# Kernel tuning notes

Hardware: AMD Instinct MI355X
Metric: run time of the kernel (lower is better)

Reference implementation:

```python
import jax, jax.numpy as jnp
import numpy as np

SMOOTH = 6.0
EPS = 1e-8
NEG_SLOPE = 0.1

def setup_inputs() -> dict:
    key = jax.random.key(0)
    k1, k2 = jax.random.split(key)
    im = jax.random.normal(k1, (8192, 1024), dtype=jnp.float32)
    aud = jax.random.normal(k2, (8192, 1024), dtype=jnp.float32)
    return {"im": im, "aud": aud}

def _l2norm(x, dim=1):
    norm = jnp.sqrt(jnp.sum(x * x, axis=dim, keepdims=True)) + EPS
    return x / norm

def reference(im, aud):
    # scores: [N, M]
    scores = im @ aud.T
    s = jax.nn.leaky_relu(scores, NEG_SLOPE)
    # row path: l2norm over dim=1, scaled softmax over last dim
    s1 = jax.nn.softmax(_l2norm(s, dim=1) * SMOOTH, axis=-1)          # [N, M]
    # col path: transpose, l2norm over dim=1 (rows of [M, N]), softmax
    s2 = jax.nn.softmax(_l2norm(s.T, dim=1) * SMOOTH, axis=-1)        # [M, N]
    im_rec = s1 @ aud   # [N, D]
    aud_rec = s2 @ im   # [M, D]
    return (im_rec, aud_rec)
```

## Files before the change

### kernel.cpp

```cpp
#include <hip/hip_runtime.h>
#include <stdint.h>
#include <stddef.h>

#define NTOK 8192
#define DDIM 1024

#define WS_F 202375168ull
#define WS_C2048 135266304ull
#define WS_C1024 101711872ull
#define WS_C512   84934656ull

using f16   = _Float16;
using f16x8 = __attribute__((ext_vector_type(8))) _Float16;
using f32x4 = __attribute__((ext_vector_type(4))) float;

__device__ __forceinline__ void gload16(const void* g, void* l) {
  __builtin_amdgcn_global_load_lds(
      (const __attribute__((address_space(1))) void*)g,
      (__attribute__((address_space(3))) void*)l, 16, 0, 0);
}

__device__ __forceinline__ void stage_tile(const f16* __restrict__ src, int ld,
                                           int row0, int k0, f16* lds, int tid) {
#pragma unroll
  for (int base = 0; base < 1024; base += 256) {
    const int cl = base + tid;
    const int r = cl >> 3;
    const int cs = (cl & 7) ^ (r & 7);
    gload16(src + (size_t)(row0 + r) * ld + k0 + cs * 8, (char*)lds + (size_t)cl * 16);
  }
}

__device__ __forceinline__ f16x8 frag_ld(const f16* lds, int r, int kc) {
  const int c = kc ^ (r & 7);
  return *(const f16x8*)((const char*)lds + r * 128 + c * 16);
}

__device__ __forceinline__ int xcd_swz(int bid, int nwg) {
  return (bid & 7) * (nwg >> 3) + (bid >> 3);
}

__global__ void prep_kernel(const float* __restrict__ inA, const float* __restrict__ inB,
                            f16* __restrict__ nA, f16* __restrict__ tA,
                            f16* __restrict__ nB, f16* __restrict__ tB) {
  const float* in = blockIdx.z ? inB : inA;
  f16* nrm = blockIdx.z ? nB : nA;
  f16* trp = blockIdx.z ? tB : tA;
  __shared__ float tile[32][33];
  const int c0 = blockIdx.x * 32;
  const int r0 = blockIdx.y * 32;
  const int tx = threadIdx.x, ty = threadIdx.y;
#pragma unroll
  for (int rr = 0; rr < 32; rr += 8) {
    const int r = r0 + rr + ty;
    const float v = in[(size_t)r * DDIM + c0 + tx];
    tile[rr + ty][tx] = v;
    nrm[(size_t)r * DDIM + c0 + tx] = (f16)v;
  }
  __syncthreads();
#pragma unroll
  for (int rr = 0; rr < 32; rr += 8) {
    trp[(size_t)(c0 + rr + ty) * NTOK + r0 + tx] = (f16)tile[tx][rr + ty];
  }
}

#define GEMM_CORE_R(Asrc, lda, Bsrc, ldb, K0, K1)                                     \
  for (int k0 = (K0); k0 < (K1); k0 += 64) {                                          \
    __syncthreads();                                                                  \
    stage_tile(Asrc, lda, row0, k0, Al, tid);                                         \
    stage_tile(Bsrc, ldb, col0, k0, Bl, tid);                                         \
    __syncthreads();                                                                  \
    _Pragma("unroll")                                                                 \
    for (int kk = 0; kk < 2; ++kk) {                                                  \
      f16x8 a[4], b[4];                                                               \
      _Pragma("unroll")                                                               \
      for (int m = 0; m < 4; ++m) a[m] = frag_ld(Al, wr + m * 16 + l15, kk * 4 + lg); \
      _Pragma("unroll")                                                               \
      for (int n = 0; n < 4; ++n) b[n] = frag_ld(Bl, wc + n * 16 + l15, kk * 4 + lg); \
      _Pragma("unroll")                                                               \
      for (int m = 0; m < 4; ++m)                                                     \
        _Pragma("unroll")                                                             \
        for (int n = 0; n < 4; ++n)                                                   \
          acc[m][n] = __builtin_amdgcn_mfma_f32_16x16x32_f16(a[m], b[n], acc[m][n], 0, 0, 0); \
    }                                                                                 \
  }
#define GEMM_CORE(Asrc, lda, Bsrc, ldb, KLEN) GEMM_CORE_R(Asrc, lda, Bsrc, ldb, 0, KLEN)

__global__ __launch_bounds__(256, 2)
void sgemm_kernel(const f16* __restrict__ A, const f16* __restrict__ B,
                  float* __restrict__ row_ss, float* __restrict__ col_ss,
                  f16* __restrict__ Sb) {
  __shared__ __align__(16) char smem[128 * 136 * 2];
  f16* Al = (f16*)smem;
  f16* Bl = (f16*)(smem + 16384);
  f16* RP = (f16*)smem;
  const int tid = threadIdx.x;
  const int lane = tid & 63, wid = tid >> 6;
  const int wr = (wid >> 1) * 64, wc = (wid & 1) * 64;
  const int l15 = lane & 15, lg = lane >> 4;
  const int swz = xcd_swz(blockIdx.x, 4096);
  const int row0 = (swz & 63) * 128, col0 = (swz >> 6) * 128;
  f32x4 acc[4][4];
#pragma unroll
  for (int m = 0; m < 4; ++m)
#pragma unroll
    for (int n = 0; n < 4; ++n) acc[m][n] = (f32x4){0.f, 0.f, 0.f, 0.f};

  GEMM_CORE(A, DDIM, B, DDIM, DDIM)

#pragma unroll
  for (int m = 0; m < 4; ++m)
#pragma unroll
    for (int n = 0; n < 4; ++n)
#pragma unroll
      for (int q = 0; q < 4; ++q) {
        const float v = acc[m][n][q];
        acc[m][n][q] = v > 0.f ? v : 0.1f * v;
      }
  float cpart[4] = {0.f, 0.f, 0.f, 0.f};
#pragma unroll
  for (int m = 0; m < 4; ++m) {
    float rpart[4] = {0.f, 0.f, 0.f, 0.f};
#pragma unroll
    for (int n = 0; n < 4; ++n) {
#pragma unroll
      for (int q = 0; q < 4; ++q) {
        const float v2 = acc[m][n][q] * acc[m][n][q];
        rpart[q] += v2;
        cpart[n] += v2;
      }
    }
#pragma unroll
    for (int q = 0; q < 4; ++q) {
      float s = rpart[q];
      s += __shfl_xor(s, 1, 64);
      s += __shfl_xor(s, 2, 64);
      s += __shfl_xor(s, 4, 64);
      s += __shfl_xor(s, 8, 64);
      if (l15 == 0) atomicAdd(&row_ss[row0 + wr + m * 16 + lg * 4 + q], s);
    }
  }
#pragma unroll
  for (int n = 0; n < 4; ++n) {
    float s = cpart[n];
    s += __shfl_xor(s, 16, 64);
    s += __shfl_xor(s, 32, 64);
    if (lg == 0) atomicAdd(&col_ss[col0 + wc + n * 16 + l15], s);
  }
  __syncthreads();
#pragma unroll
  for (int m = 0; m < 4; ++m)
#pragma unroll
    for (int n = 0; n < 4; ++n)
#pragma unroll
      for (int q = 0; q < 4; ++q)
        RP[(wr + m * 16 + lg * 4 + q) * 136 + wc + n * 16 + l15] = (f16)acc[m][n][q];
  __syncthreads();
#pragma unroll
  for (int it = 0; it < 8; ++it) {
    const int r = it * 16 + (tid >> 4);
    const int c8 = (tid & 15) * 8;
    *(f16x8*)(Sb + (size_t)(row0 + r) * NTOK + col0 + c8) = *(const f16x8*)(RP + r * 136 + c8);
  }
}

__global__ void scales_kernel(const float* __restrict__ row_ss, const float* __restrict__ col_ss,
                              float* __restrict__ s1p, float* __restrict__ s2p) {
  const int i = blockIdx.x * 256 + threadIdx.x;
  const float c = 6.0f * 1.4426950408889634f;
  s1p[i] = c / (sqrtf(row_ss[i]) + 1e-8f);
  s2p[i] = c / (sqrtf(col_ss[i]) + 1e-8f);
}

__global__ __launch_bounds__(256)
void texp_kernel(const f16* __restrict__ Sb, f16* __restrict__ P2c,
                 const float* __restrict__ s2p, float* __restrict__ Z2, int j0c) {
  __shared__ float T[128][33];
  const int t = threadIdx.x;
  const int i0 = blockIdx.x * 128;
  const int jc = blockIdx.y * 32;
  const int jg = j0c + jc;
#pragma unroll
  for (int it = 0; it < 2; ++it) {
    const int lin = it * 256 + t;
    const int r = lin >> 2, c8 = (lin & 3) * 8;
    const f16x8 v = *(const f16x8*)(Sb + (size_t)(i0 + r) * NTOK + jg + c8);
#pragma unroll
    for (int e = 0; e < 8; ++e) T[r][c8 + e] = (float)v[e];
  }
  __syncthreads();
#pragma unroll
  for (int it = 0; it < 2; ++it) {
    const int lin = it * 256 + t;
    const int j = lin >> 4, ic = lin & 15;
    const float s = s2p[jg + j];
    f16x8 o;
    float sum = 0.f;
#pragma unroll
    for (int e = 0; e < 8; ++e) {
      const float p = exp2f(T[ic * 8 + e][j] * s);
      o[e] = (f16)p;
      sum += (float)o[e];
    }
    *(f16x8*)(P2c + (size_t)(jc + j) * NTOK + i0 + ic * 8) = o;
    sum += __shfl_xor(sum, 1, 64);
    sum += __shfl_xor(sum, 2, 64);
    sum += __shfl_xor(sum, 4, 64);
    sum += __shfl_xor(sum, 8, 64);
    if ((t & 15) == 0) atomicAdd(&Z2[jg + j], sum);
  }
}

__global__ __launch_bounds__(256, 2)
void gemm2_kernel(const f16* __restrict__ A, const f16* __restrict__ Bt,
                  float* __restrict__ C) {
  __shared__ __align__(16) f16 Al[128 * 64];
  __shared__ __align__(16) f16 Bl[128 * 64];
  const int tid = threadIdx.x;
  const int lane = tid & 63, wid = tid >> 6;
  const int wr = (wid >> 1) * 64, wc = (wid & 1) * 64;
  const int l15 = lane & 15, lg = lane >> 4;
  const int swz = xcd_swz(blockIdx.x, 512);
  const int tile = swz >> 2, kq = swz & 3;
  const int row0 = (tile >> 3) * 128, col0 = (tile & 7) * 128;
  f32x4 acc[4][4];
#pragma unroll
  for (int m = 0; m < 4; ++m)
#pragma unroll
    for (int n = 0; n < 4; ++n) acc[m][n] = (f32x4){0.f, 0.f, 0.f, 0.f};

  GEMM_CORE_R(A, NTOK, Bt, NTOK, kq * 2048, kq * 2048 + 2048)

#pragma unroll
  for (int m = 0; m < 4; ++m)
#pragma unroll
    for (int n = 0; n < 4; ++n) {
      const int ccol = col0 + wc + n * 16 + l15;
#pragma unroll
      for (int q = 0; q < 4; ++q) {
        const int crow = row0 + wr + m * 16 + lg * 4 + q;
        atomicAdd(&C[(size_t)crow * DDIM + ccol], acc[m][n][q]);
      }
    }
}

__global__ __launch_bounds__(256, 8)
void expz_kernel(f16* __restrict__ M, const float* __restrict__ s1p, float* __restrict__ Z1) {
  const int wid = threadIdx.x >> 6, lane = threadIdx.x & 63;
  const int row = blockIdx.x * 4 + wid;
  const float s = s1p[row];
  f16* rp = M + (size_t)row * NTOK;
  float acc = 0.f;
#pragma unroll
  for (int c = 0; c < 16; ++c) {
    f16x8* p = (f16x8*)(rp + (c * 64 + lane) * 8);
    f16x8 v = *p;
    f16x8 o;
#pragma unroll
    for (int e = 0; e < 8; ++e) {
      o[e] = (f16)exp2f((float)v[e] * s);
      acc += (float)o[e];
    }
    *p = o;
  }
#pragma unroll
  for (int d = 1; d < 64; d <<= 1) acc += __shfl_xor(acc, d, 64);
  if (lane == 0) Z1[row] = acc;
}

__global__ __launch_bounds__(256, 2)
void pass1_kernel(const f16* __restrict__ A, const f16* __restrict__ B,
                  float* __restrict__ row_ss, float* __restrict__ col_ss) {
  __shared__ __align__(16) f16 Al[128 * 64];
  __shared__ __align__(16) f16 Bl[128 * 64];
  const int tid = threadIdx.x;
  const int lane = tid & 63, wid = tid >> 6;
  const int wr = (wid >> 1) * 64, wc = (wid & 1) * 64;
  const int l15 = lane & 15, lg = lane >> 4;
  const int swz = xcd_swz(blockIdx.x, 4096);
  const int row0 = (swz & 63) * 128, col0 = (swz >> 6) * 128;
  f32x4 acc[4][4];
#pragma unroll
  for (int m = 0; m < 4; ++m)
#pragma unroll
    for (int n = 0; n < 4; ++n) acc[m][n] = (f32x4){0.f, 0.f, 0.f, 0.f};

  GEMM_CORE(A, DDIM, B, DDIM, DDIM)

  float cpart[4] = {0.f, 0.f, 0.f, 0.f};
#pragma unroll
  for (int m = 0; m < 4; ++m) {
    float rpart[4] = {0.f, 0.f, 0.f, 0.f};
#pragma unroll
    for (int n = 0; n < 4; ++n) {
#pragma unroll
      for (int q = 0; q < 4; ++q) {
        float v = acc[m][n][q];
        v = v > 0.f ? v : 0.1f * v;
        const float v2 = v * v;
        rpart[q] += v2;
        cpart[n] += v2;
      }
    }
#pragma unroll
    for (int q = 0; q < 4; ++q) {
      float s = rpart[q];
      s += __shfl_xor(s, 1, 64);
      s += __shfl_xor(s, 2, 64);
      s += __shfl_xor(s, 4, 64);
      s += __shfl_xor(s, 8, 64);
      if (l15 == 0) atomicAdd(&row_ss[row0 + wr + m * 16 + lg * 4 + q], s);
    }
  }
#pragma unroll
  for (int n = 0; n < 4; ++n) {
    float s = cpart[n];
    s += __shfl_xor(s, 16, 64);
    s += __shfl_xor(s, 32, 64);
    if (lg == 0) atomicAdd(&col_ss[col0 + wc + n * 16 + l15], s);
  }
}

__global__ __launch_bounds__(256, 2)
void pass2c_kernel(const f16* __restrict__ A, const f16* __restrict__ B,
                   const float* __restrict__ s1p, const float* __restrict__ s2p,
                   f16* __restrict__ P1c, f16* __restrict__ P2c,
                   float* __restrict__ Z1, float* __restrict__ Z2, int j0, int CHJ) {
  __shared__ __align__(16) char smem[128 * 136 * 2];
  f16* Al = (f16*)smem;
  f16* Bl = (f16*)(smem + 16384);
  f16* RP = (f16*)smem;
  const int tid = threadIdx.x;
  const int lane = tid & 63, wid = tid >> 6;
  const int wr = (wid >> 1) * 64, wc = (wid & 1) * 64;
  const int l15 = lane & 15, lg = lane >> 4;
  const int row0 = blockIdx.x * 128;
  const int col0loc = blockIdx.y * 128;
  const int col0 = j0 + col0loc;
  f32x4 acc[4][4];
#pragma unroll
  for (int m = 0; m < 4; ++m)
#pragma unroll
    for (int n = 0; n < 4; ++n) acc[m][n] = (f32x4){0.f, 0.f, 0.f, 0.f};

  GEMM_CORE(A, DDIM, B, DDIM, DDIM)

#pragma unroll
  for (int m = 0; m < 4; ++m)
#pragma unroll
    for (int n = 0; n < 4; ++n)
#pragma unroll
      for (int q = 0; q < 4; ++q) {
        const float v = acc[m][n][q];
        acc[m][n][q] = v > 0.f ? v : 0.1f * v;
      }
  float sr[4][4], sc[4];
#pragma unroll
  for (int m = 0; m < 4; ++m)
#pragma unroll
    for (int q = 0; q < 4; ++q) sr[m][q] = s1p[row0 + wr + m * 16 + lg * 4 + q];
#pragma unroll
  for (int n = 0; n < 4; ++n) sc[n] = s2p[col0 + wc + n * 16 + l15];

  __syncthreads();
#pragma unroll
  for (int m = 0; m < 4; ++m)
#pragma unroll
    for (int n = 0; n < 4; ++n)
#pragma unroll
      for (int q = 0; q < 4; ++q) {
        const float p = exp2f(acc[m][n][q] * sr[m][q]);
        RP[(wr + m * 16 + lg * 4 + q) * 136 + wc + n * 16 + l15] = (f16)p;
      }
  __syncthreads();
#pragma unroll
  for (int it = 0; it < 8; ++it) {
    const int r = it * 16 + (tid >> 4);
    const int c8 = (tid & 15) * 8;
    const f16x8 v = *(const f16x8*)(RP + r * 136 + c8);
    float s = 0.f;
#pragma unroll
    for (int e = 0; e < 8; ++e) s += (float)v[e];
    *(f16x8*)(P1c + (size_t)(row0 + r) * CHJ + col0loc + c8) = v;
    s += __shfl_xor(s, 1, 64);
    s += __shfl_xor(s, 2, 64);
    s += __shfl_xor(s, 4, 64);
    s += __shfl_xor(s, 8, 64);
    if ((tid & 15) == 0) atomicAdd(&Z1[row0 + r], s);
  }
  __syncthreads();
#pragma unroll
  for (int m = 0; m < 4; ++m)
#pragma unroll
    for (int n = 0; n < 4; ++n)
#pragma unroll
      for (int q = 0; q < 4; ++q) {
        const float p = exp2f(acc[m][n][q] * sc[n]);
        RP[(wc + n * 16 + l15) * 136 + wr + m * 16 + lg * 4 + q] = (f16)p;
      }
  __syncthreads();
#pragma unroll
  for (int it = 0; it < 8; ++it) {
    const int r = it * 16 + (tid >> 4);
    const int c8 = (tid & 15) * 8;
    const f16x8 v = *(const f16x8*)(RP + r * 136 + c8);
    float s = 0.f;
#pragma unroll
    for (int e = 0; e < 8; ++e) s += (float)v[e];
    *(f16x8*)(P2c + (size_t)(col0loc + r) * NTOK + row0 + c8) = v;
    s += __shfl_xor(s, 1, 64);
    s += __shfl_xor(s, 2, 64);
    s += __shfl_xor(s, 4, 64);
    s += __shfl_xor(s, 8, 64);
    if ((tid & 15) == 0) atomicAdd(&Z2[col0 + r], s);
  }
}

__global__ __launch_bounds__(256, 2)
void gemm_out_kernel(const f16* __restrict__ A, int lda,
                     const f16* __restrict__ Bt, int ldb,
                     float* __restrict__ C, int K, int beta, int nwg) {
  __shared__ __align__(16) f16 Al[128 * 64];
  __shared__ __align__(16) f16 Bl[128 * 64];
  const int tid = threadIdx.x;
  const int lane = tid & 63, wid = tid >> 6;
  const int wr = (wid >> 1) * 64, wc = (wid & 1) * 64;
  const int l15 = lane & 15, lg = lane >> 4;
  const int swz = xcd_swz(blockIdx.x, nwg);
  const int row0 = (swz >> 3) * 128, col0 = (swz & 7) * 128;
  f32x4 acc[4][4];
#pragma unroll
  for (int m = 0; m < 4; ++m)
#pragma unroll
    for (int n = 0; n < 4; ++n) acc[m][n] = (f32x4){0.f, 0.f, 0.f, 0.f};

  GEMM_CORE(A, lda, Bt, ldb, K)

#pragma unroll
  for (int m = 0; m < 4; ++m)
#pragma unroll
    for (int n = 0; n < 4; ++n) {
      const int ccol = col0 + wc + n * 16 + l15;
#pragma unroll
      for (int q = 0; q < 4; ++q) {
        const int crow = row0 + wr + m * 16 + lg * 4 + q;
        const size_t idx = (size_t)crow * DDIM + ccol;
        const float v = acc[m][n][q];
        C[idx] = beta ? C[idx] + v : v;
      }
    }
}

__global__ void norm_kernel(float* __restrict__ out, const float* __restrict__ Z1,
                            const float* __restrict__ Z2) {
  const size_t idx = (size_t)blockIdx.x * 256 + threadIdx.x;
  const size_t e = idx * 4;
  const size_t half = (size_t)NTOK * DDIM;
  const float* Z = (e < half) ? Z1 : Z2;
  const int r = (int)((e >> 10) & (NTOK - 1));
  const float inv = 1.0f / Z[r];
  f32x4* o = (f32x4*)out;
  f32x4 v = o[idx];
  v.x *= inv; v.y *= inv; v.z *= inv; v.w *= inv;
  o[idx] = v;
}

__global__ void fill_kernel(float* __restrict__ out, float v, size_t n) {
  const size_t i = (size_t)blockIdx.x * 256 + threadIdx.x;
  if (i < n) out[i] = v;
}

extern "C" void kernel_launch(void* const* d_in, const int* in_sizes, int n_in,
                              void* d_out, int out_size, void* d_ws, size_t ws_size,
                              hipStream_t stream) {
  const float* im = (const float*)d_in[0];
  const float* aud = (const float*)d_in[1];
  float* out = (float*)d_out;
  char* ws = (char*)d_ws;

  f16* im_h  = (f16*)(ws);
  f16* aud_h = (f16*)(ws + (size_t)16777216);
  f16* imT   = (f16*)(ws + (size_t)33554432);
  f16* audT  = (f16*)(ws + (size_t)50331648);
  float* row_ss = (float*)(ws + (size_t)67108864);
  float* col_ss = (float*)(ws + (size_t)67108864 + 32768);
  float* Z1     = (float*)(ws + (size_t)67108864 + 65536);
  float* Z2     = (float*)(ws + (size_t)67108864 + 98304);
  float* s1p    = (float*)(ws + (size_t)67108864 + 131072);
  float* s2p    = (float*)(ws + (size_t)67108864 + 163840);

  if (ws_size >= WS_F) {
    f16* Sb  = (f16*)(ws + (size_t)68157440);
    f16* P2c = (f16*)(ws);

    hipMemsetAsync(row_ss, 0, 2 * NTOK * sizeof(float), stream);
    hipMemsetAsync(Z2, 0, NTOK * sizeof(float), stream);
    hipMemsetAsync(out + (size_t)NTOK * DDIM, 0, (size_t)NTOK * DDIM * 4, stream);
    prep_kernel<<<dim3(32, 256, 2), dim3(32, 8), 0, stream>>>(im, aud, im_h, imT, aud_h, audT);
    sgemm_kernel<<<4096, 256, 0, stream>>>(im_h, aud_h, row_ss, col_ss, Sb);
    scales_kernel<<<NTOK / 256, 256, 0, stream>>>(row_ss, col_ss, s1p, s2p);
    for (int c = 0; c < 4; ++c) {
      const int j0c = c * 2048;
      texp_kernel<<<dim3(64, 64), 256, 0, stream>>>(Sb, P2c, s2p, Z2, j0c);
      gemm2_kernel<<<512, 256, 0, stream>>>(P2c, imT,
                                            out + (size_t)NTOK * DDIM + (size_t)j0c * DDIM);
    }
    expz_kernel<<<NTOK / 4, 256, 0, stream>>>(Sb, s1p, Z1);
    gemm_out_kernel<<<512, 256, 0, stream>>>(Sb, NTOK, audT, NTOK, out, NTOK, 0, 512);
    norm_kernel<<<16384, 256, 0, stream>>>(out, Z1, Z2);
  } else if (ws_size >= WS_C512) {
    const int CHJ = (ws_size >= WS_C2048) ? 2048 : (ws_size >= WS_C1024) ? 1024 : 512;
    f16* P1c = (f16*)(ws + (size_t)68157440);
    f16* P2c = (f16*)(ws + (size_t)68157440 + (size_t)NTOK * CHJ * 2);

    hipMemsetAsync(row_ss, 0, 2 * NTOK * sizeof(float), stream);
    hipMemsetAsync(Z1, 0, NTOK * sizeof(float), stream);
    hipMemsetAsync(Z2, 0, NTOK * sizeof(float), stream);
    prep_kernel<<<dim3(32, 256, 2), dim3(32, 8), 0, stream>>>(im, aud, im_h, imT, aud_h, audT);
    pass1_kernel<<<4096, 256, 0, stream>>>(im_h, aud_h, row_ss, col_ss);
    scales_kernel<<<NTOK / 256, 256, 0, stream>>>(row_ss, col_ss, s1p, s2p);
    const int nchunk = NTOK / CHJ;
    for (int cj = 0; cj < nchunk; ++cj) {
      const int j0 = cj * CHJ;
      pass2c_kernel<<<dim3(64, CHJ / 128), 256, 0, stream>>>(im_h, aud_h, s1p, s2p, P1c, P2c,
                                                             Z1, Z2, j0, CHJ);
      gemm_out_kernel<<<512, 256, 0, stream>>>(P1c, CHJ, audT + j0, NTOK, out, CHJ, cj > 0, 512);
      gemm_out_kernel<<<(CHJ / 128) * 8, 256, 0, stream>>>(P2c, NTOK, imT, NTOK,
                                                           out + (size_t)NTOK * DDIM +
                                                               (size_t)j0 * DDIM,
                                                           NTOK, 0, (CHJ / 128) * 8);
    }
    norm_kernel<<<16384, 256, 0, stream>>>(out, Z1, Z2);
  } else {
    fill_kernel<<<(2u * NTOK * DDIM + 255) / 256, 256, 0, stream>>>(out, 1234.5f,
                                                                    (size_t)2 * NTOK * DDIM);
  }
}
```

Before: 842.6 us.

## Fuse row exp into transpose-exp kernel and fold normalization into GEMM epilogues

```diff
diff --git a/kernel.cpp b/kernel.cpp
--- a/kernel.cpp
+++ b/kernel.cpp
@@ -173,47 +173,64 @@
 }
 
 __global__ __launch_bounds__(256)
-void texp_kernel(const f16* __restrict__ Sb, f16* __restrict__ P2c,
-                 const float* __restrict__ s2p, float* __restrict__ Z2, int j0c) {
-  __shared__ float T[128][33];
+void texp2_kernel(f16* __restrict__ Sb, f16* __restrict__ P2c,
+                  const float* __restrict__ s1p, const float* __restrict__ s2p,
+                  float* __restrict__ Z1, float* __restrict__ Z2, int j0c) {
+  __shared__ f16 T[64][130];
   const int t = threadIdx.x;
   const int i0 = blockIdx.x * 128;
-  const int jc = blockIdx.y * 32;
-  const int jg = j0c + jc;
-#pragma unroll
-  for (int it = 0; it < 2; ++it) {
+  const int jl = blockIdx.y * 64;
+  const int jg = j0c + jl;
+#pragma unroll
+  for (int it = 0; it < 4; ++it) {
     const int lin = it * 256 + t;
-    const int r = lin >> 2, c8 = (lin & 3) * 8;
-    const f16x8 v = *(const f16x8*)(Sb + (size_t)(i0 + r) * NTOK + jg + c8);
-#pragma unroll
-    for (int e = 0; e < 8; ++e) T[r][c8 + e] = (float)v[e];
-  }
-  __syncthreads();
-#pragma unroll
-  for (int it = 0; it < 2; ++it) {
+    const int r = lin >> 3;
+    const int c8 = (lin & 7) * 8;
+    f16* addr = Sb + (size_t)(i0 + r) * NTOK + jg + c8;
+    const f16x8 v = *(const f16x8*)addr;
+    const float s1 = s1p[i0 + r];
+    f16x8 o;
+    float zp = 0.f;
+#pragma unroll
+    for (int e = 0; e < 8; ++e) {
+      const float x = (float)v[e];
+      T[c8 + e][r] = v[e];
+      o[e] = (f16)exp2f(x * s1);
+      zp += (float)o[e];
+    }
+    *(f16x8*)addr = o;
+    zp += __shfl_xor(zp, 1, 64);
+    zp += __shfl_xor(zp, 2, 64);
+    zp += __shfl_xor(zp, 4, 64);
+    if ((t & 7) == 0) atomicAdd(&Z1[i0 + r], zp);
+  }
+  __syncthreads();
+#pragma unroll
+  for (int it = 0; it < 4; ++it) {
     const int lin = it * 256 + t;
-    const int j = lin >> 4, ic = lin & 15;
-    const float s = s2p[jg + j];
+    const int jj = lin >> 4;
+    const int iof = (lin & 15) * 8;
+    const float s2 = s2p[jg + jj];
     f16x8 o;
-    float sum = 0.f;
+    float zp = 0.f;
 #pragma unroll
     for (int e = 0; e < 8; ++e) {
-      const float p = exp2f(T[ic * 8 + e][j] * s);
-      o[e] = (f16)p;
-      sum += (float)o[e];
-    }
-    *(f16x8*)(P2c + (size_t)(jc + j) * NTOK + i0 + ic * 8) = o;
-    sum += __shfl_xor(sum, 1, 64);
-    sum += __shfl_xor(sum, 2, 64);
-    sum += __shfl_xor(sum, 4, 64);
-    sum += __shfl_xor(sum, 8, 64);
-    if ((t & 15) == 0) atomicAdd(&Z2[jg + j], sum);
+      const float x = (float)T[jj][iof + e];
+      o[e] = (f16)exp2f(x * s2);
+      zp += (float)o[e];
+    }
+    *(f16x8*)(P2c + (size_t)(jl + jj) * NTOK + i0 + iof) = o;
+    zp += __shfl_xor(zp, 1, 64);
+    zp += __shfl_xor(zp, 2, 64);
+    zp += __shfl_xor(zp, 4, 64);
+    zp += __shfl_xor(zp, 8, 64);
+    if ((t & 15) == 0) atomicAdd(&Z2[jg + jj], zp);
   }
 }
 
 __global__ __launch_bounds__(256, 2)
 void gemm2_kernel(const f16* __restrict__ A, const f16* __restrict__ Bt,
-                  float* __restrict__ C) {
+                  float* __restrict__ C, const float* __restrict__ Zrow) {
   __shared__ __align__(16) f16 Al[128 * 64];
   __shared__ __align__(16) f16 Bl[128 * 64];
   const int tid = threadIdx.x;
@@ -239,33 +256,9 @@
 #pragma unroll
       for (int q = 0; q < 4; ++q) {
         const int crow = row0 + wr + m * 16 + lg * 4 + q;
-        atomicAdd(&C[(size_t)crow * DDIM + ccol], acc[m][n][q]);
-      }
-    }
-}
-
-__global__ __launch_bounds__(256, 8)
-void expz_kernel(f16* __restrict__ M, const float* __restrict__ s1p, float* __restrict__ Z1) {
-  const int wid = threadIdx.x >> 6, lane = threadIdx.x & 63;
-  const int row = blockIdx.x * 4 + wid;
-  const float s = s1p[row];
-  f16* rp = M + (size_t)row * NTOK;
-  float acc = 0.f;
-#pragma unroll
-  for (int c = 0; c < 16; ++c) {
-    f16x8* p = (f16x8*)(rp + (c * 64 + lane) * 8);
-    f16x8 v = *p;
-    f16x8 o;
-#pragma unroll
-    for (int e = 0; e < 8; ++e) {
-      o[e] = (f16)exp2f((float)v[e] * s);
-      acc += (float)o[e];
-    }
-    *p = o;
-  }
-#pragma unroll
-  for (int d = 1; d < 64; d <<= 1) acc += __shfl_xor(acc, d, 64);
-  if (lane == 0) Z1[row] = acc;
+        atomicAdd(&C[(size_t)crow * DDIM + ccol], acc[m][n][q] / Zrow[crow]);
+      }
+    }
 }
 
 __global__ __launch_bounds__(256, 2)
@@ -419,7 +412,8 @@
 __global__ __launch_bounds__(256, 2)
 void gemm_out_kernel(const f16* __restrict__ A, int lda,
                      const f16* __restrict__ Bt, int ldb,
-                     float* __restrict__ C, int K, int beta, int nwg) {
+                     float* __restrict__ C, int K, int beta, int nwg,
+                     const float* __restrict__ Zrow) {
   __shared__ __align__(16) f16 Al[128 * 64];
   __shared__ __align__(16) f16 Bl[128 * 64];
   const int tid = threadIdx.x;
@@ -445,7 +439,8 @@
       for (int q = 0; q < 4; ++q) {
         const int crow = row0 + wr + m * 16 + lg * 4 + q;
         const size_t idx = (size_t)crow * DDIM + ccol;
-        const float v = acc[m][n][q];
+        float v = acc[m][n][q];
+        if (Zrow) v /= Zrow[crow];
         C[idx] = beta ? C[idx] + v : v;
       }
     }
@@ -494,28 +489,26 @@
     f16* P2c = (f16*)(ws);
 
     hipMemsetAsync(row_ss, 0, 2 * NTOK * sizeof(float), stream);
-    hipMemsetAsync(Z2, 0, NTOK * sizeof(float), stream);
+    hipMemsetAsync(Z1, 0, 2 * NTOK * sizeof(float), stream);
     hipMemsetAsync(out + (size_t)NTOK * DDIM, 0, (size_t)NTOK * DDIM * 4, stream);
     prep_kernel<<<dim3(32, 256, 2), dim3(32, 8), 0, stream>>>(im, aud, im_h, imT, aud_h, audT);
     sgemm_kernel<<<4096, 256, 0, stream>>>(im_h, aud_h, row_ss, col_ss, Sb);
     scales_kernel<<<NTOK / 256, 256, 0, stream>>>(row_ss, col_ss, s1p, s2p);
     for (int c = 0; c < 4; ++c) {
       const int j0c = c * 2048;
-      texp_kernel<<<dim3(64, 64), 256, 0, stream>>>(Sb, P2c, s2p, Z2, j0c);
+      texp2_kernel<<<dim3(64, 32), 256, 0, stream>>>(Sb, P2c, s1p, s2p, Z1, Z2, j0c);
       gemm2_kernel<<<512, 256, 0, stream>>>(P2c, imT,
-                                            out + (size_t)NTOK * DDIM + (size_t)j0c * DDIM);
-    }
-    expz_kernel<<<NTOK / 4, 256, 0, stream>>>(Sb, s1p, Z1);
-    gemm_out_kernel<<<512, 256, 0, stream>>>(Sb, NTOK, audT, NTOK, out, NTOK, 0, 512);
-    norm_kernel<<<16384, 256, 0, stream>>>(out, Z1, Z2);
+                                            out + (size_t)NTOK * DDIM + (size_t)j0c * DDIM,
+                                            Z2 + j0c);
+    }
+    gemm_out_kernel<<<512, 256, 0, stream>>>(Sb, NTOK, audT, NTOK, out, NTOK, 0, 512, Z1);
   } else if (ws_size >= WS_C512) {
     const int CHJ = (ws_size >= WS_C2048) ? 2048 : (ws_size >= WS_C1024) ? 1024 : 512;
     f16* P1c = (f16*)(ws + (size_t)68157440);
     f16* P2c = (f16*)(ws + (size_t)68157440 + (size_t)NTOK * CHJ * 2);
 
     hipMemsetAsync(row_ss, 0, 2 * NTOK * sizeof(float), stream);
-    hipMemsetAsync(Z1, 0, NTOK * sizeof(float), stream);
-    hipMemsetAsync(Z2, 0, NTOK * sizeof(float), stream);
+    hipMemsetAsync(Z1, 0, 2 * NTOK * sizeof(float), stream);
     prep_kernel<<<dim3(32, 256, 2), dim3(32, 8), 0, stream>>>(im, aud, im_h, imT, aud_h, audT);
     pass1_kernel<<<4096, 256, 0, stream>>>(im_h, aud_h, row_ss, col_ss);
     scales_kernel<<<NTOK / 256, 256, 0, stream>>>(row_ss, col_ss, s1p, s2p);
@@ -524,11 +517,12 @@
       const int j0 = cj * CHJ;
       pass2c_kernel<<<dim3(64, CHJ / 128), 256, 0, stream>>>(im_h, aud_h, s1p, s2p, P1c, P2c,
                                                              Z1, Z2, j0, CHJ);
-      gemm_out_kernel<<<512, 256, 0, stream>>>(P1c, CHJ, audT + j0, NTOK, out, CHJ, cj > 0, 512);
+      gemm_out_kernel<<<512, 256, 0, stream>>>(P1c, CHJ, audT + j0, NTOK, out, CHJ, cj > 0, 512,
+                                               nullptr);
       gemm_out_kernel<<<(CHJ / 128) * 8, 256, 0, stream>>>(P2c, NTOK, imT, NTOK,
                                                            out + (size_t)NTOK * DDIM +
                                                                (size_t)j0 * DDIM,
-                                                           NTOK, 0, (CHJ / 128) * 8);
+                                                           NTOK, 0, (CHJ / 128) * 8, nullptr);
     }
     norm_kernel<<<16384, 256, 0, stream>>>(out, Z1, Z2);
   } else {
```

Measured after the change: 805.4 us. -4.4%, faster.
